# Performance work log

Hardware: AMD Instinct MI355X
Metric: run time of the kernel (lower is better)

The kernel has to match this reference:

```python
import jax, jax.numpy as jnp
import numpy as np

IN, OUT, R, ALPHA = 4096, 4096, 32, 32
SCALE = ALPHA / R

def setup_inputs() -> dict:
    key = jax.random.key(0)
    k1, k2, k3, k4, k5 = jax.random.split(key, 5)
    x = jax.random.normal(k1, (4, 2048, IN), dtype=jnp.float32)
    weight = jax.random.normal(k2, (OUT, IN), dtype=jnp.float32) * 0.02
    bias = jax.random.normal(k3, (OUT,), dtype=jnp.float32) * 0.02
    A = jax.random.normal(k4, (OUT, R), dtype=jnp.float32) * 0.01
    # original init is zeros; use small randn so the LoRA path is nontrivial
    B = jax.random.normal(k5, (IN, R), dtype=jnp.float32) * 0.01
    return {"x": x, "weight": weight, "bias": bias, "A": A, "B": B}

def reference(x, weight, bias, A, B):
    # delta_w = A @ B.T * (alpha/r); y = x @ (W + delta_w).T + bias
    delta_w = (A @ B.T) * SCALE            # [out, in]
    w_eff = weight + delta_w
    return jnp.einsum('bsi,oi->bso', x, w_eff) + bias
```

## Files before the change

### kernel.cpp

```cpp
#include <hip/hip_runtime.h>

#define IN_DIM 4096
#define OUT_DIM 4096
#define M_DIM 8192
#define RANK 32
#define BK 64
#define NT (IN_DIM / BK)

typedef __bf16 bf16x8 __attribute__((ext_vector_type(8)));
typedef float f32x4 __attribute__((ext_vector_type(4)));

__device__ __forceinline__ unsigned short f2bf(float f) {
  unsigned u = __builtin_bit_cast(unsigned, f);
  u += 0x7FFF + ((u >> 16) & 1);
  return (unsigned short)(u >> 16);
}

__global__ void prep_x_kernel(const float* __restrict__ X,
                              unsigned short* __restrict__ Xb) {
  const int stride = gridDim.x * blockDim.x;
  const int total4 = (M_DIM * IN_DIM) / 4;
  for (int i = blockIdx.x * blockDim.x + threadIdx.x; i < total4; i += stride) {
    const float4 v = reinterpret_cast<const float4*>(X)[i];
    ushort4 o;
    o.x = f2bf(v.x); o.y = f2bf(v.y); o.z = f2bf(v.z); o.w = f2bf(v.w);
    reinterpret_cast<ushort4*>(Xb)[i] = o;
  }
}

__global__ __launch_bounds__(256) void prep_w_kernel(
    const float* __restrict__ W, const float* __restrict__ A,
    const float* __restrict__ B, unsigned short* __restrict__ Wb) {
  __shared__ unsigned short sA[128][40];
  __shared__ unsigned short sB[128][40];
  const int tid  = threadIdx.x;
  const int lane = tid & 63;
  const int wid  = tid >> 6;
  const int wr   = wid >> 1, wc = wid & 1;
  const int li   = lane & 15, kg = lane >> 4;
  const int bRow = blockIdx.y * 128;
  const int bCol = blockIdx.x * 128;

  for (int i = tid; i < 128 * 8; i += 256) {
    const int r = i >> 3, q = i & 7;
    const float4 va = reinterpret_cast<const float4*>(A + (size_t)(bRow + r) * RANK)[q];
    ushort4 oa;
    oa.x = f2bf(va.x); oa.y = f2bf(va.y); oa.z = f2bf(va.z); oa.w = f2bf(va.w);
    *reinterpret_cast<ushort4*>(&sA[r][q * 4]) = oa;
    const float4 vb = reinterpret_cast<const float4*>(B + (size_t)(bCol + r) * RANK)[q];
    ushort4 ob;
    ob.x = f2bf(vb.x); ob.y = f2bf(vb.y); ob.z = f2bf(vb.z); ob.w = f2bf(vb.w);
    *reinterpret_cast<ushort4*>(&sB[r][q * 4]) = ob;
  }
  __syncthreads();

  bf16x8 af[4], bq[4];
#pragma unroll
  for (int m = 0; m < 4; ++m)
    af[m] = *reinterpret_cast<const bf16x8*>(&sA[wr * 64 + m * 16 + li][kg * 8]);
#pragma unroll
  for (int n = 0; n < 4; ++n)
    bq[n] = *reinterpret_cast<const bf16x8*>(&sB[wc * 64 + n * 16 + li][kg * 8]);

  f32x4 acc[4][4];
#pragma unroll
  for (int m = 0; m < 4; ++m)
#pragma unroll
    for (int n = 0; n < 4; ++n) {
      acc[m][n] = f32x4{0.f, 0.f, 0.f, 0.f};
      acc[m][n] = __builtin_amdgcn_mfma_f32_16x16x32_bf16(af[m], bq[n], acc[m][n], 0, 0, 0);
    }

#pragma unroll
  for (int m = 0; m < 4; ++m) {
#pragma unroll
    for (int n = 0; n < 4; ++n) {
      const int col = bCol + wc * 64 + n * 16 + li;
#pragma unroll
      for (int j = 0; j < 4; ++j) {
        const int row = bRow + wr * 64 + m * 16 + kg * 4 + j;
        const size_t idx = (size_t)row * IN_DIM + col;
        Wb[idx] = f2bf(W[idx] + acc[m][n][j]);
      }
    }
  }
}

__global__ __launch_bounds__(512, 2) void gemm_kernel(
    const unsigned short* __restrict__ Xb, const unsigned short* __restrict__ Wb,
    const float* __restrict__ bias, float* __restrict__ Y) {
  __shared__ unsigned short lds[8][8192];
  const int tid  = threadIdx.x;
  const int lane = tid & 63;
  const int wid  = tid >> 6;
  const int wr   = wid >> 2;
  const int wc   = wid & 3;
  const int li   = lane & 15, kg = lane >> 4;

  const int bid = blockIdx.x;
  const int swz = (bid & 7) * 64 + (bid >> 3);
  const int bx  = swz & 15;
  const int by  = swz >> 4;
  const int bRow = by * 256, bCol = bx * 256;

  const int kcS = (tid & 7) ^ ((tid >> 3) & 7);
  const unsigned short* srcA[2][2];
  const unsigned short* srcB[2][2];
#pragma unroll
  for (int h = 0; h < 2; ++h)
#pragma unroll
    for (int l = 0; l < 2; ++l) {
      const int gA = l * 128 + h * 64 + (tid >> 3);
      const int gB = (l * 2 + (tid >> 8)) * 64 + h * 32 + ((tid >> 3) & 31);
      srcA[h][l] = Xb + (size_t)(bRow + gA) * IN_DIM + kcS * 8;
      srcB[h][l] = Wb + (size_t)(bCol + gB) * IN_DIM + kcS * 8;
    }
  char* const ldsRaw = (char*)&lds[0][0];

#define GLD(src, dstoff)                                                       \
  __builtin_amdgcn_global_load_lds(                                            \
      (const __attribute__((address_space(1))) unsigned int*)(src),            \
      (__attribute__((address_space(3))) unsigned int*)(ldsRaw + (dstoff)),    \
      16, 0, 0)
#define STAGE_A(s, h)                                                          \
  do {                                                                         \
    const int q_ = (((s) & 1) << 2) + (h);                                     \
    GLD(srcA[h][0] + (s) * BK, q_ * 16384 + tid * 16);                         \
    GLD(srcA[h][1] + (s) * BK, q_ * 16384 + 8192 + tid * 16);                  \
  } while (0)
#define STAGE_B(s, h)                                                          \
  do {                                                                         \
    const int q_ = (((s) & 1) << 2) + 2 + (h);                                 \
    GLD(srcB[h][0] + (s) * BK, q_ * 16384 + tid * 16);                         \
    GLD(srcB[h][1] + (s) * BK, q_ * 16384 + 8192 + tid * 16);                  \
  } while (0)
#define BAR() __builtin_amdgcn_s_barrier()

  const int rowAoff = (wr * 64 + li) * 64;
  const int rowBoff = (wc * 32 + li) * 64;
  int kx[2];
  kx[0] = ((0 * 4 + kg) ^ (li & 7)) * 8;
  kx[1] = ((1 * 4 + kg) ^ (li & 7)) * 8;

  bf16x8 af[4][2], bq[4][2];
  f32x4 acc[8][4];
#pragma unroll
  for (int m = 0; m < 8; ++m)
#pragma unroll
    for (int n = 0; n < 4; ++n) acc[m][n] = f32x4{0.f, 0.f, 0.f, 0.f};

#define RD_A(ms_)                                                              \
  do {                                                                         \
    const unsigned short* b_ = &lds[(dcur << 2) + (ms_)][0] + rowAoff;         \
    _Pragma("unroll") for (int mq = 0; mq < 4; ++mq)                           \
      _Pragma("unroll") for (int ks = 0; ks < 2; ++ks)                         \
        af[mq][ks] =                                                           \
            *reinterpret_cast<const bf16x8*>(b_ + mq * 1024 + kx[ks]);         \
  } while (0)
#define RD_B(ns_)                                                              \
  do {                                                                         \
    const unsigned short* b_ = &lds[(dcur << 2) + 2 + (ns_)][0] + rowBoff;     \
    _Pragma("unroll") for (int nq = 0; nq < 2; ++nq)                           \
      _Pragma("unroll") for (int ks = 0; ks < 2; ++ks)                         \
        bq[(ns_) * 2 + nq][ks] =                                               \
            *reinterpret_cast<const bf16x8*>(b_ + nq * 1024 + kx[ks]);         \
  } while (0)
#define MM(ms_, ns_)                                                           \
  do {                                                                         \
    __builtin_amdgcn_s_setprio(1);                                             \
    _Pragma("unroll") for (int mq = 0; mq < 4; ++mq)                           \
      _Pragma("unroll") for (int nq = 0; nq < 2; ++nq)                         \
        _Pragma("unroll") for (int ks = 0; ks < 2; ++ks)                       \
          acc[(ms_) * 4 + mq][(ns_) * 2 + nq] =                                \
              __builtin_amdgcn_mfma_f32_16x16x32_bf16(                         \
                  af[mq][ks], bq[(ns_) * 2 + nq][ks],                          \
                  acc[(ms_) * 4 + mq][(ns_) * 2 + nq], 0, 0, 0);               \
    __builtin_amdgcn_s_setprio(0);                                             \
  } while (0)

  STAGE_A(0, 0); STAGE_A(0, 1); STAGE_B(0, 0); STAGE_B(0, 1);
  STAGE_A(1, 0); STAGE_B(1, 0); STAGE_A(1, 1);
  asm volatile("s_waitcnt vmcnt(6)" ::: "memory");
  BAR();

  for (int t = 0; t < NT; ++t) {
    const int dcur = t & 1;
    const bool st1 = (t + 1 < NT), st2 = (t + 2 < NT);
    if (st1) STAGE_B(t + 1, 1);
    RD_A(0); RD_B(0);
    BAR();
    MM(0, 0);
    BAR();
    if (st2) STAGE_A(t + 2, 0);
    RD_B(1);
    BAR();
    MM(0, 1);
    BAR();
    if (st2) STAGE_B(t + 2, 0);
    RD_A(1);
    BAR();
    MM(1, 0);
    BAR();
    if (st2) STAGE_A(t + 2, 1);
    BAR();
    MM(1, 1);
    if (st2) asm volatile("s_waitcnt vmcnt(6)" ::: "memory");
    else     asm volatile("s_waitcnt vmcnt(0)" ::: "memory");
    BAR();
  }
#undef GLD
#undef STAGE_A
#undef STAGE_B
#undef RD_A
#undef RD_B
#undef MM
#undef BAR

#pragma unroll
  for (int nf = 0; nf < 4; ++nf) {
    const int col = bCol + wc * 64 + nf * 16 + li;
    const float bv = bias[col];
#pragma unroll
    for (int mf = 0; mf < 8; ++mf) {
      const int row0 = bRow + wr * 128 + mf * 16 + kg * 4;
#pragma unroll
      for (int j = 0; j < 4; ++j)
        Y[(size_t)(row0 + j) * OUT_DIM + col] = acc[mf][nf][j] + bv;
    }
  }
}

extern "C" void kernel_launch(void* const* d_in, const int* in_sizes, int n_in,
                              void* d_out, int out_size, void* d_ws, size_t ws_size,
                              hipStream_t stream) {
  const float* x    = (const float*)d_in[0];
  const float* w    = (const float*)d_in[1];
  const float* bias = (const float*)d_in[2];
  const float* A    = (const float*)d_in[3];
  const float* B    = (const float*)d_in[4];
  float* y = (float*)d_out;

  const size_t xb_bytes = (size_t)M_DIM * IN_DIM * 2;
  const size_t wb_bytes = (size_t)OUT_DIM * IN_DIM * 2;
  if (ws_size < xb_bytes + wb_bytes) return;

  unsigned short* Xb = (unsigned short*)d_ws;
  unsigned short* Wb = (unsigned short*)((char*)d_ws + xb_bytes);

  prep_x_kernel<<<2048, 256, 0, stream>>>(x, Xb);
  prep_w_kernel<<<dim3(IN_DIM / 128, OUT_DIM / 128), 256, 0, stream>>>(w, A, B, Wb);
  gemm_kernel<<<(M_DIM / 256) * (OUT_DIM / 256), 512, 0, stream>>>(Xb, Wb, bias, y);
}
```

Before: 292.5 us.

## Use 32x32x16 MFMA in GEMM and merge the two prep kernels into one launch

After: 318.1 us. 8.8% more time.

```diff
diff --git a/kernel.cpp b/kernel.cpp
--- a/kernel.cpp
+++ b/kernel.cpp
@@ -9,6 +9,7 @@
 
 typedef __bf16 bf16x8 __attribute__((ext_vector_type(8)));
 typedef float f32x4 __attribute__((ext_vector_type(4)));
+typedef float f32x16 __attribute__((ext_vector_type(16)));
 
 __device__ __forceinline__ unsigned short f2bf(float f) {
   unsigned u = __builtin_bit_cast(unsigned, f);
@@ -16,30 +17,31 @@
   return (unsigned short)(u >> 16);
 }
 
-__global__ void prep_x_kernel(const float* __restrict__ X,
-                              unsigned short* __restrict__ Xb) {
-  const int stride = gridDim.x * blockDim.x;
-  const int total4 = (M_DIM * IN_DIM) / 4;
-  for (int i = blockIdx.x * blockDim.x + threadIdx.x; i < total4; i += stride) {
-    const float4 v = reinterpret_cast<const float4*>(X)[i];
-    ushort4 o;
-    o.x = f2bf(v.x); o.y = f2bf(v.y); o.z = f2bf(v.z); o.w = f2bf(v.w);
-    reinterpret_cast<ushort4*>(Xb)[i] = o;
-  }
-}
-
-__global__ __launch_bounds__(256) void prep_w_kernel(
+__global__ __launch_bounds__(256) void prep_kernel(
+    const float* __restrict__ X, unsigned short* __restrict__ Xb,
     const float* __restrict__ W, const float* __restrict__ A,
     const float* __restrict__ B, unsigned short* __restrict__ Wb) {
+  const int tid = threadIdx.x;
+  if (blockIdx.x >= 1024) {
+    const int idx0 = (blockIdx.x - 1024) * 256 + tid;
+    const int stride = 512 * 256;
+    const int total4 = (M_DIM * IN_DIM) / 4;
+    for (int i = idx0; i < total4; i += stride) {
+      const float4 v = reinterpret_cast<const float4*>(X)[i];
+      ushort4 o;
+      o.x = f2bf(v.x); o.y = f2bf(v.y); o.z = f2bf(v.z); o.w = f2bf(v.w);
+      reinterpret_cast<ushort4*>(Xb)[i] = o;
+    }
+    return;
+  }
   __shared__ unsigned short sA[128][40];
   __shared__ unsigned short sB[128][40];
-  const int tid  = threadIdx.x;
   const int lane = tid & 63;
   const int wid  = tid >> 6;
   const int wr   = wid >> 1, wc = wid & 1;
   const int li   = lane & 15, kg = lane >> 4;
-  const int bRow = blockIdx.y * 128;
-  const int bCol = blockIdx.x * 128;
+  const int bRow = (blockIdx.x >> 5) * 128;
+  const int bCol = (blockIdx.x & 31) * 128;
 
   for (int i = tid; i < 128 * 8; i += 256) {
     const int r = i >> 3, q = i & 7;
@@ -95,7 +97,9 @@
   const int wid  = tid >> 6;
   const int wr   = wid >> 2;
   const int wc   = wid & 3;
-  const int li   = lane & 15, kg = lane >> 4;
+  const int l31  = lane & 31;
+  const int hf   = lane >> 5;
+  const int l7   = lane & 7;
 
   const int bid = blockIdx.x;
   const int swz = (bid & 7) * 64 + (bid >> 3);
@@ -136,45 +140,42 @@
   } while (0)
 #define BAR() __builtin_amdgcn_s_barrier()
 
-  const int rowAoff = (wr * 64 + li) * 64;
-  const int rowBoff = (wc * 32 + li) * 64;
-  int kx[2];
-  kx[0] = ((0 * 4 + kg) ^ (li & 7)) * 8;
-  kx[1] = ((1 * 4 + kg) ^ (li & 7)) * 8;
-
-  bf16x8 af[4][2], bq[4][2];
-  f32x4 acc[8][4];
-#pragma unroll
-  for (int m = 0; m < 8; ++m)
-#pragma unroll
-    for (int n = 0; n < 4; ++n) acc[m][n] = f32x4{0.f, 0.f, 0.f, 0.f};
+  const int rowAoff = (wr * 64 + l31) * 64;
+  const int rowBoff = (wc * 32 + l31) * 64;
+  int kxx[4];
+#pragma unroll
+  for (int ks = 0; ks < 4; ++ks) kxx[ks] = ((ks * 2 + hf) ^ l7) * 8;
+
+  bf16x8 af[2][4], bq[2][4];
+  f32x16 acc[4][2];
+#pragma unroll
+  for (int m = 0; m < 4; ++m)
+#pragma unroll
+    for (int n = 0; n < 2; ++n)
+#pragma unroll
+      for (int j = 0; j < 16; ++j) acc[m][n][j] = 0.f;
 
 #define RD_A(ms_)                                                              \
   do {                                                                         \
     const unsigned short* b_ = &lds[(dcur << 2) + (ms_)][0] + rowAoff;         \
-    _Pragma("unroll") for (int mq = 0; mq < 4; ++mq)                           \
-      _Pragma("unroll") for (int ks = 0; ks < 2; ++ks)                         \
+    _Pragma("unroll") for (int mq = 0; mq < 2; ++mq)                           \
+      _Pragma("unroll") for (int ks = 0; ks < 4; ++ks)                         \
         af[mq][ks] =                                                           \
-            *reinterpret_cast<const bf16x8*>(b_ + mq * 1024 + kx[ks]);         \
+            *reinterpret_cast<const bf16x8*>(b_ + mq * 2048 + kxx[ks]);        \
   } while (0)
 #define RD_B(ns_)                                                              \
   do {                                                                         \
     const unsigned short* b_ = &lds[(dcur << 2) + 2 + (ns_)][0] + rowBoff;     \
-    _Pragma("unroll") for (int nq = 0; nq < 2; ++nq)                           \
-      _Pragma("unroll") for (int ks = 0; ks < 2; ++ks)                         \
-        bq[(ns_) * 2 + nq][ks] =                                               \
-            *reinterpret_cast<const bf16x8*>(b_ + nq * 1024 + kx[ks]);         \
+    _Pragma("unroll") for (int ks = 0; ks < 4; ++ks)                           \
+      bq[ns_][ks] = *reinterpret_cast<const bf16x8*>(b_ + kxx[ks]);            \
   } while (0)
 #define MM(ms_, ns_)                                                           \
   do {                                                                         \
     __builtin_amdgcn_s_setprio(1);                                             \
-    _Pragma("unroll") for (int mq = 0; mq < 4; ++mq)                           \
-      _Pragma("unroll") for (int nq = 0; nq < 2; ++nq)                         \
-        _Pragma("unroll") for (int ks = 0; ks < 2; ++ks)                       \
-          acc[(ms_) * 4 + mq][(ns_) * 2 + nq] =                                \
-              __builtin_amdgcn_mfma_f32_16x16x32_bf16(                         \
-                  af[mq][ks], bq[(ns_) * 2 + nq][ks],                          \
-                  acc[(ms_) * 4 + mq][(ns_) * 2 + nq], 0, 0, 0);               \
+    _Pragma("unroll") for (int mq = 0; mq < 2; ++mq)                           \
+      _Pragma("unroll") for (int ks = 0; ks < 4; ++ks)                         \
+        acc[(ms_) * 2 + mq][ns_] = __builtin_amdgcn_mfma_f32_32x32x16_bf16(    \
+            af[mq][ks], bq[ns_][ks], acc[(ms_) * 2 + mq][ns_], 0, 0, 0);       \
     __builtin_amdgcn_s_setprio(0);                                             \
   } while (0)
 
@@ -217,15 +218,17 @@
 #undef BAR
 
 #pragma unroll
-  for (int nf = 0; nf < 4; ++nf) {
-    const int col = bCol + wc * 64 + nf * 16 + li;
+  for (int nf = 0; nf < 2; ++nf) {
+    const int col = bCol + wc * 64 + nf * 32 + l31;
     const float bv = bias[col];
 #pragma unroll
-    for (int mf = 0; mf < 8; ++mf) {
-      const int row0 = bRow + wr * 128 + mf * 16 + kg * 4;
-#pragma unroll
-      for (int j = 0; j < 4; ++j)
-        Y[(size_t)(row0 + j) * OUT_DIM + col] = acc[mf][nf][j] + bv;
+    for (int mf = 0; mf < 4; ++mf) {
+      const int rbase = bRow + wr * 128 + mf * 32 + hf * 4;
+#pragma unroll
+      for (int j = 0; j < 16; ++j) {
+        const int row = rbase + (j & 3) + 8 * (j >> 2);
+        Y[(size_t)row * OUT_DIM + col] = acc[mf][nf][j] + bv;
+      }
     }
   }
 }
@@ -247,7 +250,6 @@
   unsigned short* Xb = (unsigned short*)d_ws;
   unsigned short* Wb = (unsigned short*)((char*)d_ws + xb_bytes);
 
-  prep_x_kernel<<<2048, 256, 0, stream>>>(x, Xb);
-  prep_w_kernel<<<dim3(IN_DIM / 128, OUT_DIM / 128), 256, 0, stream>>>(w, A, B, Wb);
+  prep_kernel<<<1536, 256, 0, stream>>>(x, Xb, w, A, B, Wb);
   gemm_kernel<<<(M_DIM / 256) * (OUT_DIM / 256), 512, 0, stream>>>(Xb, Wb, bias, y);
 }
```

## Merge prep kernels into one launch and reschedule GEMM stage pipeline

Applied to the files above, without the earlier changes.

Result: faster. 276.9 us, median of 3 (-5.3%).

```diff
diff --git a/kernel.cpp b/kernel.cpp
--- a/kernel.cpp
+++ b/kernel.cpp
@@ -16,30 +16,31 @@
   return (unsigned short)(u >> 16);
 }
 
-__global__ void prep_x_kernel(const float* __restrict__ X,
-                              unsigned short* __restrict__ Xb) {
-  const int stride = gridDim.x * blockDim.x;
-  const int total4 = (M_DIM * IN_DIM) / 4;
-  for (int i = blockIdx.x * blockDim.x + threadIdx.x; i < total4; i += stride) {
-    const float4 v = reinterpret_cast<const float4*>(X)[i];
-    ushort4 o;
-    o.x = f2bf(v.x); o.y = f2bf(v.y); o.z = f2bf(v.z); o.w = f2bf(v.w);
-    reinterpret_cast<ushort4*>(Xb)[i] = o;
-  }
-}
-
-__global__ __launch_bounds__(256) void prep_w_kernel(
+__global__ __launch_bounds__(256) void prep_kernel(
+    const float* __restrict__ X, unsigned short* __restrict__ Xb,
     const float* __restrict__ W, const float* __restrict__ A,
     const float* __restrict__ B, unsigned short* __restrict__ Wb) {
+  const int tid = threadIdx.x;
+  if (blockIdx.x >= 1024) {
+    const int idx0 = (blockIdx.x - 1024) * 256 + tid;
+    const int stride = 512 * 256;
+    const int total4 = (M_DIM * IN_DIM) / 4;
+    for (int i = idx0; i < total4; i += stride) {
+      const float4 v = reinterpret_cast<const float4*>(X)[i];
+      ushort4 o;
+      o.x = f2bf(v.x); o.y = f2bf(v.y); o.z = f2bf(v.z); o.w = f2bf(v.w);
+      reinterpret_cast<ushort4*>(Xb)[i] = o;
+    }
+    return;
+  }
   __shared__ unsigned short sA[128][40];
   __shared__ unsigned short sB[128][40];
-  const int tid  = threadIdx.x;
   const int lane = tid & 63;
   const int wid  = tid >> 6;
   const int wr   = wid >> 1, wc = wid & 1;
   const int li   = lane & 15, kg = lane >> 4;
-  const int bRow = blockIdx.y * 128;
-  const int bCol = blockIdx.x * 128;
+  const int bRow = (blockIdx.x >> 5) * 128;
+  const int bCol = (blockIdx.x & 31) * 128;
 
   for (int i = tid; i < 128 * 8; i += 256) {
     const int r = i >> 3, q = i & 7;
@@ -178,35 +179,33 @@
     __builtin_amdgcn_s_setprio(0);                                             \
   } while (0)
 
-  STAGE_A(0, 0); STAGE_A(0, 1); STAGE_B(0, 0); STAGE_B(0, 1);
-  STAGE_A(1, 0); STAGE_B(1, 0); STAGE_A(1, 1);
-  asm volatile("s_waitcnt vmcnt(6)" ::: "memory");
+  STAGE_A(0, 0); STAGE_B(0, 0); STAGE_A(0, 1); STAGE_B(0, 1);
+  STAGE_A(1, 0); STAGE_B(1, 0);
+  asm volatile("s_waitcnt vmcnt(4)" ::: "memory");
   BAR();
 
   for (int t = 0; t < NT; ++t) {
     const int dcur = t & 1;
     const bool st1 = (t + 1 < NT), st2 = (t + 2 < NT);
-    if (st1) STAGE_B(t + 1, 1);
+    if (st1) { STAGE_B(t + 1, 1); STAGE_A(t + 1, 1); }
     RD_A(0); RD_B(0);
     BAR();
     MM(0, 0);
-    BAR();
+    RD_B(1);
+    BAR();
+    MM(0, 1);
     if (st2) STAGE_A(t + 2, 0);
-    RD_B(1);
-    BAR();
-    MM(0, 1);
-    BAR();
-    if (st2) STAGE_B(t + 2, 0);
     RD_A(1);
     BAR();
     MM(1, 0);
-    BAR();
-    if (st2) STAGE_A(t + 2, 1);
+    if (st2) {
+      STAGE_B(t + 2, 0);
+      asm volatile("s_waitcnt vmcnt(4)" ::: "memory");
+    } else {
+      asm volatile("s_waitcnt vmcnt(0)" ::: "memory");
+    }
     BAR();
     MM(1, 1);
-    if (st2) asm volatile("s_waitcnt vmcnt(6)" ::: "memory");
-    else     asm volatile("s_waitcnt vmcnt(0)" ::: "memory");
-    BAR();
   }
 #undef GLD
 #undef STAGE_A
@@ -247,7 +246,6 @@
   unsigned short* Xb = (unsigned short*)d_ws;
   unsigned short* Wb = (unsigned short*)((char*)d_ws + xb_bytes);
 
-  prep_x_kernel<<<2048, 256, 0, stream>>>(x, Xb);
-  prep_w_kernel<<<dim3(IN_DIM / 128, OUT_DIM / 128), 256, 0, stream>>>(w, A, B, Wb);
+  prep_kernel<<<1536, 256, 0, stream>>>(x, Xb, w, A, B, Wb);
   gemm_kernel<<<(M_DIM / 256) * (OUT_DIM / 256), 512, 0, stream>>>(Xb, Wb, bias, y);
 }
```
